# Performance work log

Hardware: AMD Instinct MI355X
Metric: run time of the kernel (lower is better)

The kernel has to match this reference:

```python
import jax, jax.numpy as jnp
import numpy as np

B, H, W, C = 32, 112, 112, 256
RATIO = 8
HID = C // RATIO

def setup_inputs() -> dict:
    key = jax.random.key(0)
    kx, kw1, kw2 = jax.random.split(key, 3)
    x = jax.random.normal(kx, (B, H, W, C), dtype=jnp.float32)
    # he_normal: std = sqrt(2/fan_in)
    w1 = jax.random.normal(kw1, (C, HID), dtype=jnp.float32) * np.sqrt(2.0 / C)
    b1 = jnp.zeros((HID,), dtype=jnp.float32)
    w2 = jax.random.normal(kw2, (HID, C), dtype=jnp.float32) * np.sqrt(2.0 / HID)
    b2 = jnp.zeros((C,), dtype=jnp.float32)
    return {"x": x, "w1": w1, "b1": b1, "w2": w2, "b2": b2}

def _mlp(p, w1, b1, w2, b2):
    # p: [B, C] -> [B, C]
    h = jax.nn.relu(p @ w1 + b1)
    return h @ w2 + b2

def reference(x, w1, b1, w2, b2):
    avg_pool = jnp.mean(x, axis=(1, 2))  # [B, C]
    max_pool = jnp.max(x, axis=(1, 2))   # [B, C]
    scale = jax.nn.sigmoid(_mlp(avg_pool, w1, b1, w2, b2) + _mlp(max_pool, w1, b1, w2, b2))
    return x * scale[:, None, None, :]
```

## Files before the change

### kernel.cpp

```cpp
#include <hip/hip_runtime.h>
#include <math.h>

#define Bn   32
#define Hn   112
#define Wn   112
#define Cn   256
#define HWn  (Hn * Wn)
#define C4   (Cn / 4)
#define HIDn 32
#define NB1  32
#define POSB (HWn / NB1)
#define NB3  98
#define POS3 (HWn / NB3)

typedef float f4 __attribute__((ext_vector_type(4)));

__global__ __launch_bounds__(256) void pool_kernel(
    const f4* __restrict__ x4,
    float* __restrict__ psum,
    float* __restrict__ pmax)
{
    const int b   = blockIdx.y;
    const int blk = blockIdx.x;
    const int tid = threadIdx.x;
    const int c4  = tid & 63;
    const int grp = tid >> 6;

    const f4* base = x4 + ((size_t)b * HWn + (size_t)blk * POSB) * C4;

    f4 s = {0.f, 0.f, 0.f, 0.f};
    f4 m = {-3.402823466e38f, -3.402823466e38f,
            -3.402823466e38f, -3.402823466e38f};

    #pragma unroll 2
    for (int p = grp; p < POSB; p += 4) {
        f4 v = base[(size_t)p * C4 + c4];
        s += v;
        m.x = fmaxf(m.x, v.x); m.y = fmaxf(m.y, v.y);
        m.z = fmaxf(m.z, v.z); m.w = fmaxf(m.w, v.w);
    }

    __shared__ f4 ls[256];
    __shared__ f4 lm[256];
    ls[tid] = s;
    lm[tid] = m;
    __syncthreads();

    if (tid < 64) {
        f4 s0 = ls[tid], s1 = ls[tid + 64], s2 = ls[tid + 128], s3 = ls[tid + 192];
        f4 m0 = lm[tid], m1 = lm[tid + 64], m2 = lm[tid + 128], m3 = lm[tid + 192];
        f4 so = (s0 + s1) + (s2 + s3);
        f4 mo;
        mo.x = fmaxf(fmaxf(m0.x, m1.x), fmaxf(m2.x, m3.x));
        mo.y = fmaxf(fmaxf(m0.y, m1.y), fmaxf(m2.y, m3.y));
        mo.z = fmaxf(fmaxf(m0.z, m1.z), fmaxf(m2.z, m3.z));
        mo.w = fmaxf(fmaxf(m0.w, m1.w), fmaxf(m2.w, m3.w));
        f4* ps4 = (f4*)(psum + ((size_t)b * NB1 + blk) * Cn);
        f4* pm4 = (f4*)(pmax + ((size_t)b * NB1 + blk) * Cn);
        __builtin_nontemporal_store(so, &ps4[tid]);
        __builtin_nontemporal_store(mo, &pm4[tid]);
    }
}

__global__ __launch_bounds__(256) void mlp_kernel(
    const float* __restrict__ psum,
    const float* __restrict__ pmax,
    const float* __restrict__ w1,
    const float* __restrict__ b1,
    const float* __restrict__ w2,
    const float* __restrict__ b2,
    float* __restrict__ scale)
{
    const int b   = blockIdx.x;
    const int tid = threadIdx.x;

    __shared__ float avg[Cn];
    __shared__ float mx[Cn];
    __shared__ float h2[2][HIDn];

    float s = 0.f;
    float m = -3.402823466e38f;
    for (int k = 0; k < NB1; ++k) {
        s += psum[((size_t)b * NB1 + k) * Cn + tid];
        m = fmaxf(m, pmax[((size_t)b * NB1 + k) * Cn + tid]);
    }
    avg[tid] = s * (1.0f / (float)HWn);
    mx[tid]  = m;
    __syncthreads();

    if (tid < 64) {
        const int j = tid & 31;
        const int which = tid >> 5;
        const float* pool = which ? mx : avg;
        float acc = b1[j];
        for (int c = 0; c < Cn; ++c)
            acc += pool[c] * w1[c * HIDn + j];
        h2[which][j] = fmaxf(acc, 0.f);
    }
    __syncthreads();

    float acc = 2.0f * b2[tid];
    for (int j = 0; j < HIDn; ++j)
        acc += (h2[0][j] + h2[1][j]) * w2[j * Cn + tid];
    scale[(size_t)b * Cn + tid] = 1.0f / (1.0f + expf(-acc));
}

__global__ __launch_bounds__(256) void scale_kernel(
    const f4* __restrict__ x4,
    const float* __restrict__ scale,
    f4* __restrict__ out4)
{
    const int b   = (Bn - 1)  - (int)blockIdx.y;
    const int blk = (NB3 - 1) - (int)blockIdx.x;
    const int tid = threadIdx.x;
    const int c4  = tid & 63;
    const int grp = tid >> 6;

    const f4 sc = ((const f4*)(scale + (size_t)b * Cn))[c4];

    const size_t base = ((size_t)b * HWn + (size_t)blk * POS3) * C4;

    #pragma unroll 4
    for (int p = grp; p < POS3; p += 4) {
        const size_t idx = base + (size_t)p * C4 + c4;
        f4 v = x4[idx];
        v *= sc;
        __builtin_nontemporal_store(v, &out4[idx]);
    }
}

extern "C" void kernel_launch(void* const* d_in, const int* in_sizes, int n_in,
                              void* d_out, int out_size, void* d_ws, size_t ws_size,
                              hipStream_t stream) {
    const float* x  = (const float*)d_in[0];
    const float* w1 = (const float*)d_in[1];
    const float* b1 = (const float*)d_in[2];
    const float* w2 = (const float*)d_in[3];
    const float* b2 = (const float*)d_in[4];
    float* out = (float*)d_out;

    float* psum  = (float*)d_ws;
    float* pmax  = psum + (size_t)Bn * NB1 * Cn;
    float* scale = pmax + (size_t)Bn * NB1 * Cn;

    pool_kernel<<<dim3(NB1, Bn), 256, 0, stream>>>((const f4*)x, psum, pmax);
    mlp_kernel<<<Bn, 256, 0, stream>>>(psum, pmax, w1, b1, w2, b2, scale);
    scale_kernel<<<dim3(NB3, Bn), 256, 0, stream>>>((const f4*)x, scale, (f4*)out);
}
```

Before: 743.3 us.

## Fuse pool, MLP and scale into cooperative kernel processing batch chunks for cache reuse

```diff
diff --git a/kernel.cpp b/kernel.cpp
--- a/kernel.cpp
+++ b/kernel.cpp
@@ -1,5 +1,8 @@
 #include <hip/hip_runtime.h>
+#include <hip/hip_cooperative_groups.h>
 #include <math.h>
+
+namespace cg = cooperative_groups;
 
 #define Bn   32
 #define Hn   112
@@ -8,12 +11,130 @@
 #define HWn  (Hn * Wn)
 #define C4   (Cn / 4)
 #define HIDn 32
+
+#define BCH    8
+#define NCHUNK (Bn / BCH)
+#define NBF    128
+#define POSF   (HWn / NBF)
+#define GRIDF  (BCH * NBF)
+
 #define NB1  32
 #define POSB (HWn / NB1)
 #define NB3  98
 #define POS3 (HWn / NB3)
 
+#define NEG_INF (-3.402823466e38f)
+
 typedef float f4 __attribute__((ext_vector_type(4)));
+
+__global__ __launch_bounds__(256, 4) void fused_kernel(
+    const f4* __restrict__ x4,
+    const float* __restrict__ w1,
+    const float* __restrict__ b1,
+    const float* __restrict__ w2,
+    const float* __restrict__ b2,
+    f4* __restrict__ out4,
+    float* __restrict__ psum,
+    float* __restrict__ pmax,
+    float* __restrict__ scale)
+{
+    cg::grid_group grid = cg::this_grid();
+
+    const int tid     = threadIdx.x;
+    const int c4      = tid & 63;
+    const int grp     = tid >> 6;
+    const int bid     = blockIdx.x;
+    const int b_local = bid >> 7;
+    const int blk     = bid & (NBF - 1);
+
+    __shared__ f4 ls[256];
+    __shared__ f4 lm[256];
+    __shared__ float avg[Cn];
+    __shared__ float mx[Cn];
+    __shared__ float h2[2][HIDn];
+
+    for (int c = 0; c < NCHUNK; ++c) {
+        const int b = c * BCH + b_local;
+
+        {
+            const f4* base = x4 + ((size_t)b * HWn + (size_t)blk * POSF) * C4;
+            f4 s = {0.f, 0.f, 0.f, 0.f};
+            f4 m = {NEG_INF, NEG_INF, NEG_INF, NEG_INF};
+            #pragma unroll 2
+            for (int p = grp; p < POSF; p += 4) {
+                f4 v = base[(size_t)p * C4 + c4];
+                s += v;
+                m.x = fmaxf(m.x, v.x); m.y = fmaxf(m.y, v.y);
+                m.z = fmaxf(m.z, v.z); m.w = fmaxf(m.w, v.w);
+            }
+            ls[tid] = s;
+            lm[tid] = m;
+            __syncthreads();
+            if (tid < 64) {
+                f4 s0 = ls[tid], s1 = ls[tid + 64], s2 = ls[tid + 128], s3 = ls[tid + 192];
+                f4 m0 = lm[tid], m1 = lm[tid + 64], m2 = lm[tid + 128], m3 = lm[tid + 192];
+                f4 so = (s0 + s1) + (s2 + s3);
+                f4 mo;
+                mo.x = fmaxf(fmaxf(m0.x, m1.x), fmaxf(m2.x, m3.x));
+                mo.y = fmaxf(fmaxf(m0.y, m1.y), fmaxf(m2.y, m3.y));
+                mo.z = fmaxf(fmaxf(m0.z, m1.z), fmaxf(m2.z, m3.z));
+                mo.w = fmaxf(fmaxf(m0.w, m1.w), fmaxf(m2.w, m3.w));
+                f4* ps4 = (f4*)(psum + ((size_t)b * NBF + blk) * Cn);
+                f4* pm4 = (f4*)(pmax + ((size_t)b * NBF + blk) * Cn);
+                ps4[tid] = so;
+                pm4[tid] = mo;
+            }
+        }
+
+        grid.sync();
+
+        if (bid < BCH) {
+            const int bb = c * BCH + bid;
+            float s = 0.f;
+            float m = NEG_INF;
+            #pragma unroll 4
+            for (int k = 0; k < NBF; ++k) {
+                s += psum[((size_t)bb * NBF + k) * Cn + tid];
+                m = fmaxf(m, pmax[((size_t)bb * NBF + k) * Cn + tid]);
+            }
+            avg[tid] = s * (1.0f / (float)HWn);
+            mx[tid]  = m;
+            __syncthreads();
+
+            if (tid < 64) {
+                const int j = tid & 31;
+                const int which = tid >> 5;
+                const float* pool = which ? mx : avg;
+                float acc = b1[j];
+                #pragma unroll 4
+                for (int cc = 0; cc < Cn; ++cc)
+                    acc += pool[cc] * w1[cc * HIDn + j];
+                h2[which][j] = fmaxf(acc, 0.f);
+            }
+            __syncthreads();
+
+            float acc = 2.0f * b2[tid];
+            #pragma unroll
+            for (int j = 0; j < HIDn; ++j)
+                acc += (h2[0][j] + h2[1][j]) * w2[j * Cn + tid];
+            scale[(size_t)bb * Cn + tid] = 1.0f / (1.0f + expf(-acc));
+        }
+
+        grid.sync();
+
+        {
+            const f4 sc = ((const f4*)(scale + (size_t)b * Cn))[c4];
+            const size_t base = ((size_t)b * HWn + (size_t)blk * POSF) * C4;
+            #pragma unroll 2
+            for (int p = grp; p < POSF; p += 4) {
+                const size_t idx = base + (size_t)p * C4 + c4;
+                f4 v = x4[idx];
+                v *= sc;
+                __builtin_nontemporal_store(v, &out4[idx]);
+            }
+        }
+    }
+}
 
 __global__ __launch_bounds__(256) void pool_kernel(
     const f4* __restrict__ x4,
@@ -29,8 +150,7 @@
     const f4* base = x4 + ((size_t)b * HWn + (size_t)blk * POSB) * C4;
 
     f4 s = {0.f, 0.f, 0.f, 0.f};
-    f4 m = {-3.402823466e38f, -3.402823466e38f,
-            -3.402823466e38f, -3.402823466e38f};
+    f4 m = {NEG_INF, NEG_INF, NEG_INF, NEG_INF};
 
     #pragma unroll 2
     for (int p = grp; p < POSB; p += 4) {
@@ -79,7 +199,7 @@
     __shared__ float h2[2][HIDn];
 
     float s = 0.f;
-    float m = -3.402823466e38f;
+    float m = NEG_INF;
     for (int k = 0; k < NB1; ++k) {
         s += psum[((size_t)b * NB1 + k) * Cn + tid];
         m = fmaxf(m, pmax[((size_t)b * NB1 + k) * Cn + tid]);
@@ -117,7 +237,6 @@
     const int grp = tid >> 6;
 
     const f4 sc = ((const f4*)(scale + (size_t)b * Cn))[c4];
-
     const size_t base = ((size_t)b * HWn + (size_t)blk * POS3) * C4;
 
     #pragma unroll 4
@@ -139,6 +258,23 @@
     const float* b2 = (const float*)d_in[4];
     float* out = (float*)d_out;
 
+    const size_t fused_need = ((size_t)2 * Bn * NBF * Cn + (size_t)Bn * Cn) * sizeof(float);
+    if (ws_size >= fused_need) {
+        float* psum  = (float*)d_ws;
+        float* pmax  = psum + (size_t)Bn * NBF * Cn;
+        float* scale = pmax + (size_t)Bn * NBF * Cn;
+
+        const f4* x4v = (const f4*)x;
+        f4* out4v = (f4*)out;
+        void* args[] = {(void*)&x4v, (void*)&w1, (void*)&b1, (void*)&w2, (void*)&b2,
+                        (void*)&out4v, (void*)&psum, (void*)&pmax, (void*)&scale};
+        hipError_t err = hipLaunchCooperativeKernel((const void*)fused_kernel,
+                                                    dim3(GRIDF), dim3(256),
+                                                    args, 0, stream);
+        if (err == hipSuccess) return;
+        (void)hipGetLastError();
+    }
+
     float* psum  = (float*)d_ws;
     float* pmax  = psum + (size_t)Bn * NB1 * Cn;
     float* scale = pmax + (size_t)Bn * NB1 * Cn;
```

Result: slower. 1.762 ms (+137.1%).

## Split batch into chunks so scale pass re-reads input from cache

Applied to the files above, without the earlier changes.

```diff
diff --git a/kernel.cpp b/kernel.cpp
--- a/kernel.cpp
+++ b/kernel.cpp
@@ -8,32 +8,35 @@
 #define HWn  (Hn * Wn)
 #define C4   (Cn / 4)
 #define HIDn 32
-#define NB1  32
-#define POSB (HWn / NB1)
-#define NB3  98
-#define POS3 (HWn / NB3)
+
+#define BCH    8
+#define NCHUNK (Bn / BCH)
+#define NBF    128
+#define POSF   (HWn / NBF)
+
+#define NEG_INF (-3.402823466e38f)
 
 typedef float f4 __attribute__((ext_vector_type(4)));
 
-__global__ __launch_bounds__(256) void pool_kernel(
+__global__ __launch_bounds__(256) void pool_chunk(
     const f4* __restrict__ x4,
     float* __restrict__ psum,
-    float* __restrict__ pmax)
+    float* __restrict__ pmax,
+    int chunk)
 {
-    const int b   = blockIdx.y;
+    const int b   = chunk * BCH + blockIdx.y;
     const int blk = blockIdx.x;
     const int tid = threadIdx.x;
     const int c4  = tid & 63;
     const int grp = tid >> 6;
 
-    const f4* base = x4 + ((size_t)b * HWn + (size_t)blk * POSB) * C4;
+    const f4* base = x4 + ((size_t)b * HWn + (size_t)blk * POSF) * C4;
 
     f4 s = {0.f, 0.f, 0.f, 0.f};
-    f4 m = {-3.402823466e38f, -3.402823466e38f,
-            -3.402823466e38f, -3.402823466e38f};
+    f4 m = {NEG_INF, NEG_INF, NEG_INF, NEG_INF};
 
-    #pragma unroll 2
-    for (int p = grp; p < POSB; p += 4) {
+    #pragma unroll 4
+    for (int p = grp; p < POSF; p += 4) {
         f4 v = base[(size_t)p * C4 + c4];
         s += v;
         m.x = fmaxf(m.x, v.x); m.y = fmaxf(m.y, v.y);
@@ -55,23 +58,24 @@
         mo.y = fmaxf(fmaxf(m0.y, m1.y), fmaxf(m2.y, m3.y));
         mo.z = fmaxf(fmaxf(m0.z, m1.z), fmaxf(m2.z, m3.z));
         mo.w = fmaxf(fmaxf(m0.w, m1.w), fmaxf(m2.w, m3.w));
-        f4* ps4 = (f4*)(psum + ((size_t)b * NB1 + blk) * Cn);
-        f4* pm4 = (f4*)(pmax + ((size_t)b * NB1 + blk) * Cn);
-        __builtin_nontemporal_store(so, &ps4[tid]);
-        __builtin_nontemporal_store(mo, &pm4[tid]);
+        f4* ps4 = (f4*)(psum + ((size_t)b * NBF + blk) * Cn);
+        f4* pm4 = (f4*)(pmax + ((size_t)b * NBF + blk) * Cn);
+        ps4[tid] = so;
+        pm4[tid] = mo;
     }
 }
 
-__global__ __launch_bounds__(256) void mlp_kernel(
+__global__ __launch_bounds__(256) void mlp_chunk(
     const float* __restrict__ psum,
     const float* __restrict__ pmax,
     const float* __restrict__ w1,
     const float* __restrict__ b1,
     const float* __restrict__ w2,
     const float* __restrict__ b2,
-    float* __restrict__ scale)
+    float* __restrict__ scale,
+    int chunk)
 {
-    const int b   = blockIdx.x;
+    const int b   = chunk * BCH + blockIdx.x;
     const int tid = threadIdx.x;
 
     __shared__ float avg[Cn];
@@ -79,10 +83,11 @@
     __shared__ float h2[2][HIDn];
 
     float s = 0.f;
-    float m = -3.402823466e38f;
-    for (int k = 0; k < NB1; ++k) {
-        s += psum[((size_t)b * NB1 + k) * Cn + tid];
-        m = fmaxf(m, pmax[((size_t)b * NB1 + k) * Cn + tid]);
+    float m = NEG_INF;
+    #pragma unroll 4
+    for (int k = 0; k < NBF; ++k) {
+        s += psum[((size_t)b * NBF + k) * Cn + tid];
+        m = fmaxf(m, pmax[((size_t)b * NBF + k) * Cn + tid]);
     }
     avg[tid] = s * (1.0f / (float)HWn);
     mx[tid]  = m;
@@ -93,6 +98,7 @@
         const int which = tid >> 5;
         const float* pool = which ? mx : avg;
         float acc = b1[j];
+        #pragma unroll 4
         for (int c = 0; c < Cn; ++c)
             acc += pool[c] * w1[c * HIDn + j];
         h2[which][j] = fmaxf(acc, 0.f);
@@ -100,28 +106,29 @@
     __syncthreads();
 
     float acc = 2.0f * b2[tid];
+    #pragma unroll
     for (int j = 0; j < HIDn; ++j)
         acc += (h2[0][j] + h2[1][j]) * w2[j * Cn + tid];
     scale[(size_t)b * Cn + tid] = 1.0f / (1.0f + expf(-acc));
 }
 
-__global__ __launch_bounds__(256) void scale_kernel(
+__global__ __launch_bounds__(256) void scale_chunk(
     const f4* __restrict__ x4,
     const float* __restrict__ scale,
-    f4* __restrict__ out4)
+    f4* __restrict__ out4,
+    int chunk)
 {
-    const int b   = (Bn - 1)  - (int)blockIdx.y;
-    const int blk = (NB3 - 1) - (int)blockIdx.x;
+    const int b   = chunk * BCH + blockIdx.y;
+    const int blk = blockIdx.x;
     const int tid = threadIdx.x;
     const int c4  = tid & 63;
     const int grp = tid >> 6;
 
     const f4 sc = ((const f4*)(scale + (size_t)b * Cn))[c4];
-
-    const size_t base = ((size_t)b * HWn + (size_t)blk * POS3) * C4;
+    const size_t base = ((size_t)b * HWn + (size_t)blk * POSF) * C4;
 
     #pragma unroll 4
-    for (int p = grp; p < POS3; p += 4) {
+    for (int p = grp; p < POSF; p += 4) {
         const size_t idx = base + (size_t)p * C4 + c4;
         f4 v = x4[idx];
         v *= sc;
@@ -140,10 +147,15 @@
     float* out = (float*)d_out;
 
     float* psum  = (float*)d_ws;
-    float* pmax  = psum + (size_t)Bn * NB1 * Cn;
-    float* scale = pmax + (size_t)Bn * NB1 * Cn;
+    float* pmax  = psum + (size_t)Bn * NBF * Cn;
+    float* scale = pmax + (size_t)Bn * NBF * Cn;
 
-    pool_kernel<<<dim3(NB1, Bn), 256, 0, stream>>>((const f4*)x, psum, pmax);
-    mlp_kernel<<<Bn, 256, 0, stream>>>(psum, pmax, w1, b1, w2, b2, scale);
-    scale_kernel<<<dim3(NB3, Bn), 256, 0, stream>>>((const f4*)x, scale, (f4*)out);
+    const f4* x4v = (const f4*)x;
+    f4* out4v = (f4*)out;
+
+    for (int c = 0; c < NCHUNK; ++c) {
+        pool_chunk<<<dim3(NBF, BCH), 256, 0, stream>>>(x4v, psum, pmax, c);
+        mlp_chunk<<<BCH, 256, 0, stream>>>(psum, pmax, w1, b1, w2, b2, scale, c);
+        scale_chunk<<<dim3(NBF, BCH), 256, 0, stream>>>(x4v, scale, out4v, c);
+    }
 }
```

Measured after the change: 839.7 us. 1.13x slower.

## Fuse MLP into pooling kernel via last-block atomic counter

Applied to the files above, without the earlier changes.

```diff
diff --git a/kernel.cpp b/kernel.cpp
--- a/kernel.cpp
+++ b/kernel.cpp
@@ -8,17 +8,27 @@
 #define HWn  (Hn * Wn)
 #define C4   (Cn / 4)
 #define HIDn 32
+
 #define NB1  32
 #define POSB (HWn / NB1)
 #define NB3  98
 #define POS3 (HWn / NB3)
+#define CNT_STRIDE 16
+
+#define NEG_INF (-3.402823466e38f)
 
 typedef float f4 __attribute__((ext_vector_type(4)));
 
-__global__ __launch_bounds__(256) void pool_kernel(
+__global__ __launch_bounds__(256) void pool_mlp_kernel(
     const f4* __restrict__ x4,
+    const float* __restrict__ w1,
+    const float* __restrict__ b1,
+    const float* __restrict__ w2,
+    const float* __restrict__ b2,
     float* __restrict__ psum,
-    float* __restrict__ pmax)
+    float* __restrict__ pmax,
+    float* __restrict__ scale,
+    int* __restrict__ cnt)
 {
     const int b   = blockIdx.y;
     const int blk = blockIdx.x;
@@ -29,8 +39,7 @@
     const f4* base = x4 + ((size_t)b * HWn + (size_t)blk * POSB) * C4;
 
     f4 s = {0.f, 0.f, 0.f, 0.f};
-    f4 m = {-3.402823466e38f, -3.402823466e38f,
-            -3.402823466e38f, -3.402823466e38f};
+    f4 m = {NEG_INF, NEG_INF, NEG_INF, NEG_INF};
 
     #pragma unroll 2
     for (int p = grp; p < POSB; p += 4) {
@@ -57,35 +66,35 @@
         mo.w = fmaxf(fmaxf(m0.w, m1.w), fmaxf(m2.w, m3.w));
         f4* ps4 = (f4*)(psum + ((size_t)b * NB1 + blk) * Cn);
         f4* pm4 = (f4*)(pmax + ((size_t)b * NB1 + blk) * Cn);
-        __builtin_nontemporal_store(so, &ps4[tid]);
-        __builtin_nontemporal_store(mo, &pm4[tid]);
+        ps4[tid] = so;
+        pm4[tid] = mo;
     }
-}
 
-__global__ __launch_bounds__(256) void mlp_kernel(
-    const float* __restrict__ psum,
-    const float* __restrict__ pmax,
-    const float* __restrict__ w1,
-    const float* __restrict__ b1,
-    const float* __restrict__ w2,
-    const float* __restrict__ b2,
-    float* __restrict__ scale)
-{
-    const int b   = blockIdx.x;
-    const int tid = threadIdx.x;
+    __shared__ int isLast;
+    __syncthreads();
+    if (tid == 0) {
+        __threadfence();
+        int old = __hip_atomic_fetch_add(cnt + (size_t)b * CNT_STRIDE, 1,
+                                         __ATOMIC_ACQ_REL, __HIP_MEMORY_SCOPE_AGENT);
+        isLast = (old == NB1 - 1);
+    }
+    __syncthreads();
+    if (!isLast) return;
 
+    __threadfence();
     __shared__ float avg[Cn];
     __shared__ float mx[Cn];
     __shared__ float h2[2][HIDn];
 
-    float s = 0.f;
-    float m = -3.402823466e38f;
+    float ssum = 0.f;
+    float smax = NEG_INF;
+    #pragma unroll 4
     for (int k = 0; k < NB1; ++k) {
-        s += psum[((size_t)b * NB1 + k) * Cn + tid];
-        m = fmaxf(m, pmax[((size_t)b * NB1 + k) * Cn + tid]);
+        ssum += psum[((size_t)b * NB1 + k) * Cn + tid];
+        smax  = fmaxf(smax, pmax[((size_t)b * NB1 + k) * Cn + tid]);
     }
-    avg[tid] = s * (1.0f / (float)HWn);
-    mx[tid]  = m;
+    avg[tid] = ssum * (1.0f / (float)HWn);
+    mx[tid]  = smax;
     __syncthreads();
 
     if (tid < 64) {
@@ -93,6 +102,7 @@
         const int which = tid >> 5;
         const float* pool = which ? mx : avg;
         float acc = b1[j];
+        #pragma unroll 4
         for (int c = 0; c < Cn; ++c)
             acc += pool[c] * w1[c * HIDn + j];
         h2[which][j] = fmaxf(acc, 0.f);
@@ -100,6 +110,7 @@
     __syncthreads();
 
     float acc = 2.0f * b2[tid];
+    #pragma unroll
     for (int j = 0; j < HIDn; ++j)
         acc += (h2[0][j] + h2[1][j]) * w2[j * Cn + tid];
     scale[(size_t)b * Cn + tid] = 1.0f / (1.0f + expf(-acc));
@@ -117,7 +128,6 @@
     const int grp = tid >> 6;
 
     const f4 sc = ((const f4*)(scale + (size_t)b * Cn))[c4];
-
     const size_t base = ((size_t)b * HWn + (size_t)blk * POS3) * C4;
 
     #pragma unroll 4
@@ -142,8 +152,12 @@
     float* psum  = (float*)d_ws;
     float* pmax  = psum + (size_t)Bn * NB1 * Cn;
     float* scale = pmax + (size_t)Bn * NB1 * Cn;
+    int*   cnt   = (int*)(scale + (size_t)Bn * Cn);
 
-    pool_kernel<<<dim3(NB1, Bn), 256, 0, stream>>>((const f4*)x, psum, pmax);
-    mlp_kernel<<<Bn, 256, 0, stream>>>(psum, pmax, w1, b1, w2, b2, scale);
-    scale_kernel<<<dim3(NB3, Bn), 256, 0, stream>>>((const f4*)x, scale, (f4*)out);
+    hipMemsetAsync(cnt, 0, (size_t)Bn * CNT_STRIDE * sizeof(int), stream);
+
+    pool_mlp_kernel<<<dim3(NB1, Bn), 256, 0, stream>>>(
+        (const f4*)x, w1, b1, w2, b2, psum, pmax, scale, cnt);
+    scale_kernel<<<dim3(NB3, Bn), 256, 0, stream>>>(
+        (const f4*)x, scale, (f4*)out);
 }
```

Measured after the change: 823.4 us. 10.8% more time.
